# Optimization experiments

Measured on AMD Instinct MI355X. Metric: run time of the kernel, lower is better.

Reference implementation:

```python
import jax, jax.numpy as jnp
import numpy as np

N_NODES = 100000
N_EDGES = 1600000
D_IN = 128
D_HID = 128


def gcn_layer(x, src, dst, ew, W, b, n):
    """PyG GCNConv with normalize=True, add_self_loops=True (self-loop weight 1)."""
    h = x @ W  # [n, d_out]
    # degree includes self-loop weight 1.0
    deg = jax.ops.segment_sum(ew, dst, num_segments=n) + 1.0  # [n]
    dis = jnp.where(deg > 0, jax.lax.rsqrt(deg), 0.0)  # deg^{-1/2}
    norm = dis[src] * ew * dis[dst]  # [E]
    agg = jax.ops.segment_sum(norm[:, None] * h[src], dst, num_segments=n)
    # self-loop term: norm_ii = dis[i] * 1.0 * dis[i]
    agg = agg + (dis * dis)[:, None] * h
    return agg + b


def prelu(x, alpha):
    return jnp.where(x >= 0, x, alpha * x)


def setup_inputs() -> dict:
    key = jax.random.key(0)
    ks = jax.random.split(key, 12)
    x = jax.random.normal(ks[0], (N_NODES, D_IN), dtype=jnp.float32)
    edge_index = jax.random.randint(ks[1], (2, N_EDGES), 0, N_NODES, dtype=jnp.int64)
    edge_weight = jax.random.uniform(ks[2], (N_EDGES,), dtype=jnp.float32)
    s1 = 1.0 / np.sqrt(D_IN)
    s2 = 1.0 / np.sqrt(D_HID)
    params = {
        "W1": jax.random.normal(ks[3], (D_IN, D_HID), dtype=jnp.float32) * s1,
        "b1": jnp.zeros((D_HID,), dtype=jnp.float32),
        "a1": jnp.full((D_HID,), 0.25, dtype=jnp.float32),
        "W2": jax.random.normal(ks[4], (D_HID, D_HID), dtype=jnp.float32) * s2,
        "b2": jnp.zeros((D_HID,), dtype=jnp.float32),
        "a2": jnp.full((D_HID,), 0.25, dtype=jnp.float32),
        "W3": jax.random.normal(ks[5], (D_HID, D_HID), dtype=jnp.float32) * s2,
        "b3": jnp.zeros((D_HID,), dtype=jnp.float32),
        "a3": jnp.full((D_HID,), 0.25, dtype=jnp.float32),
    }
    return {"x": x, "edge_index": edge_index, "edge_weight": edge_weight, **params}


def reference(x, edge_index, edge_weight, W1, b1, a1, W2, b2, a2, W3, b3, a3):
    src, dst = edge_index[0], edge_index[1]
    n = x.shape[0]
    h = prelu(gcn_layer(x, src, dst, edge_weight, W1, b1, n), a1)
    h = prelu(gcn_layer(h, src, dst, edge_weight, W2, b2, n), a2)
    h = prelu(gcn_layer(h, src, dst, edge_weight, W3, b3, n), a3)
    return h
```

## Files before the change

kernel.cpp:

```cpp
#include <hip/hip_runtime.h>

#define N_NODES 100000
#define N_EDGES 1600000
#define D 128
#define TILE_ROWS 32
#define N_TILES (N_NODES / TILE_ROWS)
#define GEMM_BLOCKS 512
#define CHUNK 4096
#define NC ((N_EDGES + CHUNK - 1) / CHUNK)
#define NB ((N_NODES + 255) / 256)
#define HLEN (NB * NC)
#define SCAN_BLK ((HLEN + 1023) / 1024)

typedef unsigned int uint;
typedef unsigned long long u64;
typedef short short8 __attribute__((ext_vector_type(8)));
typedef float f32x4 __attribute__((ext_vector_type(4)));

__device__ inline ushort f2bf(float f) {
    union { float f; uint u; } v; v.f = f;
    uint r = v.u + 0x7fffu + ((v.u >> 16) & 1u);
    return (ushort)(r >> 16);
}
__device__ inline float bf2f(ushort b) {
    union { uint u; float f; } v; v.u = ((uint)b) << 16;
    return v.f;
}


__global__ __launch_bounds__(256) void k_hist(const int* __restrict__ dst, int* __restrict__ H) {
    __shared__ int hist[NB];
    int c = blockIdx.x;
    for (int i = threadIdx.x; i < NB; i += 256) hist[i] = 0;
    __syncthreads();
    int base = c * CHUNK;
    int lim = N_EDGES - base; if (lim > CHUNK) lim = CHUNK;
    for (int k = threadIdx.x; k < lim; k += 256)
        atomicAdd(&hist[dst[base + k] >> 8], 1);
    __syncthreads();
    for (int i = threadIdx.x; i < NB; i += 256) H[c * NB + i] = hist[i];
}

__global__ __launch_bounds__(256) void k_scanA(const int* __restrict__ H, int* __restrict__ HOFF,
                                               int* __restrict__ bsum) {
    __shared__ int sd[256];
    int t = threadIdx.x;
    int base = blockIdx.x * 1024 + t * 4;
    int v[4];
#pragma unroll
    for (int j = 0; j < 4; ++j) {
        int l = base + j;
        v[j] = (l < HLEN) ? H[(l % NC) * NB + (l / NC)] : 0;
    }
    int lsum = v[0] + v[1] + v[2] + v[3];
    sd[t] = lsum;
    __syncthreads();
    for (int off = 1; off < 256; off <<= 1) {
        int x = (t >= off) ? sd[t - off] : 0;
        __syncthreads();
        sd[t] += x;
        __syncthreads();
    }
    int excl = sd[t] - lsum;
    if (base + 0 < HLEN) HOFF[base + 0] = excl;
    if (base + 1 < HLEN) HOFF[base + 1] = excl + v[0];
    if (base + 2 < HLEN) HOFF[base + 2] = excl + v[0] + v[1];
    if (base + 3 < HLEN) HOFF[base + 3] = excl + v[0] + v[1] + v[2];
    if (t == 255) bsum[blockIdx.x] = sd[255];
}

__global__ __launch_bounds__(256) void k_scanB(int* __restrict__ bsum) {
    __shared__ int sd[256];
    int t = threadIdx.x;
    int v = (t < SCAN_BLK) ? bsum[t] : 0;
    sd[t] = v;
    __syncthreads();
    for (int off = 1; off < 256; off <<= 1) {
        int x = (t >= off) ? sd[t - off] : 0;
        __syncthreads();
        sd[t] += x;
        __syncthreads();
    }
    if (t < SCAN_BLK) bsum[t] = sd[t] - v;
}

__global__ void k_scanC(int* __restrict__ HOFF, const int* __restrict__ bsum) {
    int i = blockIdx.x * blockDim.x + threadIdx.x;
    if (i < HLEN) HOFF[i] += bsum[i >> 10];
}

__global__ __launch_bounds__(256) void k_pscat(const int* __restrict__ src, const int* __restrict__ dst,
                                               const float* __restrict__ ew, const int* __restrict__ HOFF,
                                               u64* __restrict__ tmp) {
    __shared__ int cur[NB];
    int c = blockIdx.x;
    for (int i = threadIdx.x; i < NB; i += 256) cur[i] = HOFF[i * NC + c];
    __syncthreads();
    int base = c * CHUNK;
    int lim = N_EDGES - base; if (lim > CHUNK) lim = CHUNK;
    for (int k = threadIdx.x; k < lim; k += 256) {
        int e = base + k;
        int s = src[e], t = dst[e];
        u64 q = (u64)llrintf(ew[e] * 1073741824.0f);
        int pos = atomicAdd(&cur[t >> 8], 1);
        tmp[pos] = (u64)s | ((u64)t << 17) | (q << 34);
    }
}

__global__ __launch_bounds__(256) void k_b1(const int* __restrict__ HOFF, const u64* __restrict__ tmp,
                                            float* __restrict__ dis, int* __restrict__ rowptr) {
    __shared__ int cnt[256];
    __shared__ u64 degq[256];
    __shared__ int sd[256];
    __shared__ int sbeg, send;
    int b = blockIdx.x, t = threadIdx.x;
    cnt[t] = 0; degq[t] = 0;
    if (t == 0) {
        sbeg = HOFF[b * NC];
        send = (b + 1 < NB) ? HOFF[(b + 1) * NC] : N_EDGES;
    }
    __syncthreads();
    int beg = sbeg, end = send, lo = b << 8;
    for (int e = beg + t; e < end; e += 256) {
        u64 r = tmp[e];
        int loc = (int)((r >> 17) & 0x1FFFF) - lo;
        atomicAdd(&cnt[loc], 1);
        atomicAdd(&degq[loc], r >> 34);
    }
    __syncthreads();
    int n = lo + t;
    if (n < N_NODES) {
        float deg = (float)((double)degq[t] * (1.0 / 1073741824.0));
        dis[n] = rsqrtf(deg + 1.0f);
    }
    int v = cnt[t];
    sd[t] = v;
    __syncthreads();
    for (int off = 1; off < 256; off <<= 1) {
        int x = (t >= off) ? sd[t - off] : 0;
        __syncthreads();
        sd[t] += x;
        __syncthreads();
    }
    if (n < N_NODES) rowptr[n] = beg + sd[t] - v;
    if (b == NB - 1 && t == 0) rowptr[N_NODES] = N_EDGES;
}

__global__ __launch_bounds__(256) void k_b2(const int* __restrict__ HOFF, const u64* __restrict__ tmp,
                                            const float* __restrict__ dis, const int* __restrict__ rowptr,
                                            int2* __restrict__ edges) {
    __shared__ int cur[256];
    __shared__ float disl[256];
    __shared__ int sbeg, send;
    int b = blockIdx.x, t = threadIdx.x;
    int lo = b << 8;
    int n = lo + t;
    cur[t] = (n < N_NODES) ? rowptr[n] : 0;
    disl[t] = (n < N_NODES) ? dis[n] : 0.0f;
    if (t == 0) {
        sbeg = HOFF[b * NC];
        send = (b + 1 < NB) ? HOFF[(b + 1) * NC] : N_EDGES;
    }
    __syncthreads();
    for (int e = sbeg + t; e < send; e += 256) {
        u64 r = tmp[e];
        int s = (int)(r & 0x1FFFF);
        int loc = (int)((r >> 17) & 0x1FFFF) - lo;
        float w = (float)(r >> 34) * (1.0f / 1073741824.0f);
        float coef = dis[s] * w * disl[loc];
        int pos = atomicAdd(&cur[loc], 1);
        edges[pos] = make_int2(s, __float_as_int(coef));
    }
}

__global__ void k_wsplit3(const float* __restrict__ W1, const float* __restrict__ W2,
                          const float* __restrict__ W3, ushort* __restrict__ wsp) {
    int gid = blockIdx.x * 256 + threadIdx.x;
    int l = gid >> 14;
    int i = gid & 16383;
    const float* W = (l == 0) ? W1 : (l == 1) ? W2 : W3;
    ushort* Wht = wsp + l * 32768;
    ushort* Wlt = Wht + 16384;
    int k = i >> 7, c = i & 127;
    float w = W[i];
    ushort wh = f2bf(w);
    ushort wl = f2bf(w - bf2f(wh));
    int j = k >> 3;
    int off = c * 128 + (((j ^ (c & 7)) << 3) | (k & 7));
    Wht[off] = wh;
    Wlt[off] = wl;
}

__global__ __launch_bounds__(256) void k_gemm_mfma(
    const float* __restrict__ x, const ushort* __restrict__ Wht,
    const ushort* __restrict__ Wlt, ushort* __restrict__ hb)
{
    __shared__ ushort WH[16384];
    __shared__ ushort WL[16384];
    __shared__ ushort XH[4096];
    __shared__ ushort XL[4096];

    const int tx = threadIdx.x;

    for (int i = tx; i < 2048; i += 256) {
        ((uint4*)WH)[i] = ((const uint4*)Wht)[i];
        ((uint4*)WL)[i] = ((const uint4*)Wlt)[i];
    }

    const int wv = tx >> 6;
    const int lane = tx & 63;
    const int lr = lane & 15;
    const int g = lane >> 4;
    const int c0 = wv * 32 + lr;
    const int c1 = c0 + 16;

    const int xr = (tx * 2) >> 4;
    const int xjb = (tx * 2) & 15;

    for (int tile = blockIdx.x; tile < N_TILES; tile += GEMM_BLOCKS) {
        const int row0 = tile * TILE_ROWS;
        __syncthreads();

        {
            const float* xp = x + (size_t)(row0 + xr) * D;
#pragma unroll
            for (int c = 0; c < 2; ++c) {
                int j = xjb + c;
                float4 a0 = *(const float4*)(xp + j * 8);
                float4 a1 = *(const float4*)(xp + j * 8 + 4);
                float v[8] = {a0.x, a0.y, a0.z, a0.w, a1.x, a1.y, a1.z, a1.w};
                uint4 uh, ul;
                uint* ph = (uint*)&uh; uint* pl = (uint*)&ul;
#pragma unroll
                for (int e = 0; e < 4; ++e) {
                    ushort h0 = f2bf(v[2 * e]),     h1 = f2bf(v[2 * e + 1]);
                    ushort l0 = f2bf(v[2 * e] - bf2f(h0));
                    ushort l1 = f2bf(v[2 * e + 1] - bf2f(h1));
                    ph[e] = (uint)h0 | ((uint)h1 << 16);
                    pl[e] = (uint)l0 | ((uint)l1 << 16);
                }
                int off = xr * 16 + (j ^ (xr & 7));
                ((uint4*)XH)[off] = uh;
                ((uint4*)XL)[off] = ul;
            }
        }
        __syncthreads();

        f32x4 acc[2][2] = {};
#pragma unroll
        for (int ks = 0; ks < 4; ++ks) {
            int co = ((ks * 4 + g) ^ (lr & 7)) << 3;
            short8 ah0 = *(short8*)&XH[lr * 128 + co];
            short8 ah1 = *(short8*)&XH[(16 + lr) * 128 + co];
            short8 al0 = *(short8*)&XL[lr * 128 + co];
            short8 al1 = *(short8*)&XL[(16 + lr) * 128 + co];
            short8 bh0 = *(short8*)&WH[c0 * 128 + co];
            short8 bh1 = *(short8*)&WH[c1 * 128 + co];
            short8 bl0 = *(short8*)&WL[c0 * 128 + co];
            short8 bl1 = *(short8*)&WL[c1 * 128 + co];

            acc[0][0] = __builtin_amdgcn_mfma_f32_16x16x32_bf16(ah0, bh0, acc[0][0], 0, 0, 0);
            acc[0][1] = __builtin_amdgcn_mfma_f32_16x16x32_bf16(ah0, bh1, acc[0][1], 0, 0, 0);
            acc[1][0] = __builtin_amdgcn_mfma_f32_16x16x32_bf16(ah1, bh0, acc[1][0], 0, 0, 0);
            acc[1][1] = __builtin_amdgcn_mfma_f32_16x16x32_bf16(ah1, bh1, acc[1][1], 0, 0, 0);
            acc[0][0] = __builtin_amdgcn_mfma_f32_16x16x32_bf16(al0, bh0, acc[0][0], 0, 0, 0);
            acc[0][1] = __builtin_amdgcn_mfma_f32_16x16x32_bf16(al0, bh1, acc[0][1], 0, 0, 0);
            acc[1][0] = __builtin_amdgcn_mfma_f32_16x16x32_bf16(al1, bh0, acc[1][0], 0, 0, 0);
            acc[1][1] = __builtin_amdgcn_mfma_f32_16x16x32_bf16(al1, bh1, acc[1][1], 0, 0, 0);
            acc[0][0] = __builtin_amdgcn_mfma_f32_16x16x32_bf16(ah0, bl0, acc[0][0], 0, 0, 0);
            acc[0][1] = __builtin_amdgcn_mfma_f32_16x16x32_bf16(ah0, bl1, acc[0][1], 0, 0, 0);
            acc[1][0] = __builtin_amdgcn_mfma_f32_16x16x32_bf16(ah1, bl0, acc[1][0], 0, 0, 0);
            acc[1][1] = __builtin_amdgcn_mfma_f32_16x16x32_bf16(ah1, bl1, acc[1][1], 0, 0, 0);
        }

#pragma unroll
        for (int rt = 0; rt < 2; ++rt) {
#pragma unroll
            for (int ct = 0; ct < 2; ++ct) {
                int colb = wv * 32 + ct * 16 + lr;
#pragma unroll
                for (int e = 0; e < 4; ++e) {
                    int row = row0 + rt * 16 + g * 4 + e;
                    hb[(size_t)row * D + colb] = f2bf(acc[rt][ct][e]);
                }
            }
        }
    }
}

__global__ __launch_bounds__(256) void k_gather(
    const int* __restrict__ rowptr, const int2* __restrict__ edges,
    const ushort* __restrict__ hb, const float* __restrict__ dis,
    const float* __restrict__ b, const float* __restrict__ alpha,
    float* __restrict__ out)
{
    int gid = blockIdx.x * 256 + threadIdx.x;
    int n = gid >> 6;
    if (n >= N_NODES) return;
    int lane = gid & 63;
    int q = lane >> 4;
    int c0 = (lane & 15) * 8;

    int beg = rowptr[n], end = rowptr[n + 1];
    float acc[8] = {0.f, 0.f, 0.f, 0.f, 0.f, 0.f, 0.f, 0.f};

    int e = beg + q;
    for (; e + 4 < end; e += 8) {
        int2 sc0 = edges[e];
        int2 sc1 = edges[e + 4];
        uint4 hv0 = *(const uint4*)&hb[(size_t)sc0.x * D + c0];
        uint4 hv1 = *(const uint4*)&hb[(size_t)sc1.x * D + c0];
        float ca = __int_as_float(sc0.y);
        float cb = __int_as_float(sc1.y);
#pragma unroll
        for (int j = 0; j < 4; ++j) {
            uint w0 = ((const uint*)&hv0)[j];
            uint w1 = ((const uint*)&hv1)[j];
            acc[2 * j]     = fmaf(ca, __uint_as_float(w0 << 16),         acc[2 * j]);
            acc[2 * j + 1] = fmaf(ca, __uint_as_float(w0 & 0xffff0000u), acc[2 * j + 1]);
            acc[2 * j]     = fmaf(cb, __uint_as_float(w1 << 16),         acc[2 * j]);
            acc[2 * j + 1] = fmaf(cb, __uint_as_float(w1 & 0xffff0000u), acc[2 * j + 1]);
        }
    }
    if (e < end) {
        int2 sc = edges[e];
        float c = __int_as_float(sc.y);
        uint4 hv = *(const uint4*)&hb[(size_t)sc.x * D + c0];
#pragma unroll
        for (int j = 0; j < 4; ++j) {
            uint w = ((const uint*)&hv)[j];
            acc[2 * j]     = fmaf(c, __uint_as_float(w << 16),         acc[2 * j]);
            acc[2 * j + 1] = fmaf(c, __uint_as_float(w & 0xffff0000u), acc[2 * j + 1]);
        }
    }

#pragma unroll
    for (int j = 0; j < 8; ++j) {
        acc[j] += __shfl_xor(acc[j], 16);
        acc[j] += __shfl_xor(acc[j], 32);
    }

    if (q == 0) {
        float di = dis[n];
        float d2 = di * di;
        uint4 hv = *(const uint4*)&hb[(size_t)n * D + c0];
        float r[8];
#pragma unroll
        for (int j = 0; j < 4; ++j) {
            uint w = ((const uint*)&hv)[j];
            float lo = __uint_as_float(w << 16);
            float hi = __uint_as_float(w & 0xffff0000u);
            r[2 * j]     = acc[2 * j]     + d2 * lo + b[c0 + 2 * j];
            r[2 * j + 1] = acc[2 * j + 1] + d2 * hi + b[c0 + 2 * j + 1];
        }
#pragma unroll
        for (int j = 0; j < 8; ++j) {
            float av = alpha[c0 + j];
            r[j] = r[j] >= 0.f ? r[j] : av * r[j];
        }
        *(float4*)&out[(size_t)n * D + c0]     = make_float4(r[0], r[1], r[2], r[3]);
        *(float4*)&out[(size_t)n * D + c0 + 4] = make_float4(r[4], r[5], r[6], r[7]);
    }
}


extern "C" void kernel_launch(void* const* d_in, const int* in_sizes, int n_in,
                              void* d_out, int out_size, void* d_ws, size_t ws_size,
                              hipStream_t stream) {
    const float* x   = (const float*)d_in[0];
    const int*   ei  = (const int*)d_in[1];
    const float* ew  = (const float*)d_in[2];
    const float* W1  = (const float*)d_in[3];
    const float* b1  = (const float*)d_in[4];
    const float* a1  = (const float*)d_in[5];
    const float* W2  = (const float*)d_in[6];
    const float* b2  = (const float*)d_in[7];
    const float* a2  = (const float*)d_in[8];
    const float* W3  = (const float*)d_in[9];
    const float* b3  = (const float*)d_in[10];
    const float* a3  = (const float*)d_in[11];

    const int* src = ei;
    const int* dst = ei + N_EDGES;

    float* out = (float*)d_out;

    ushort* hb    = (ushort*)d_ws;
    int2*   edges = (int2*)(hb + (size_t)N_NODES * D);
    u64*    tmp   = (u64*)(edges + N_EDGES);
    int*    H     = (int*)(tmp + N_EDGES);
    int*    HOFF  = H + HLEN;
    int*    bsum  = HOFF + HLEN;
    float*  dis   = (float*)(bsum + 256);
    int*    rowptr= (int*)(dis + N_NODES);
    ushort* wsp   = (ushort*)(rowptr + N_NODES + 2);
    ushort* Wht1 = wsp;             ushort* Wlt1 = wsp + 16384;
    ushort* Wht2 = wsp + 32768;     ushort* Wlt2 = wsp + 32768 + 16384;
    ushort* Wht3 = wsp + 65536;     ushort* Wlt3 = wsp + 65536 + 16384;

    k_wsplit3<<<192, 256, 0, stream>>>(W1, W2, W3, wsp);

    k_hist<<<NC, 256, 0, stream>>>(dst, H);
    k_scanA<<<SCAN_BLK, 256, 0, stream>>>(H, HOFF, bsum);
    k_scanB<<<1, 256, 0, stream>>>(bsum);
    k_scanC<<<(HLEN + 255) / 256, 256, 0, stream>>>(HOFF, bsum);
    k_pscat<<<NC, 256, 0, stream>>>(src, dst, ew, HOFF, tmp);
    k_b1<<<NB, 256, 0, stream>>>(HOFF, tmp, dis, rowptr);
    k_b2<<<NB, 256, 0, stream>>>(HOFF, tmp, dis, rowptr, edges);

    const int gather_blocks = (N_NODES * 64) / 256;

    k_gemm_mfma<<<GEMM_BLOCKS, 256, 0, stream>>>(x, Wht1, Wlt1, hb);
    k_gather<<<gather_blocks, 256, 0, stream>>>(rowptr, edges, hb, dis, b1, a1, out);
    k_gemm_mfma<<<GEMM_BLOCKS, 256, 0, stream>>>(out, Wht2, Wlt2, hb);
    k_gather<<<gather_blocks, 256, 0, stream>>>(rowptr, edges, hb, dis, b2, a2, out);
    k_gemm_mfma<<<GEMM_BLOCKS, 256, 0, stream>>>(out, Wht3, Wlt3, hb);
    k_gather<<<gather_blocks, 256, 0, stream>>>(rowptr, edges, hb, dis, b3, a3, out);
}
```

Baseline: 384.3 us.

## Fuse CSR build passes, pre-scale GEMM output by dis, sort edges by source bucket

Merges the two CSR-construction kernels into one, caching a block's packed edges in LDS so the temp buffer is read once when they fit. Within each destination row, edges are grouped by source-index bucket so neighbour gathers hit nearby rows of h. dis[src] is folded into the GEMM epilogue (h scaled by dis per row), which removes the random dis[s] load from edge coefficient construction and simplifies the self-loop term. The cost is larger LDS use (about 60KB) with lower occupancy, and one extra bf16 rounding of the scaled values.

```diff
diff --git a/kernel.cpp b/kernel.cpp
--- a/kernel.cpp
+++ b/kernel.cpp
@@ -11,6 +11,10 @@
 #define NB ((N_NODES + 255) / 256)
 #define HLEN (NB * NC)
 #define SCAN_BLK ((HLEN + 1023) / 1024)
+#define SB_SHIFT 13
+#define NSB 13
+#define SBP 17
+#define EBUF 5120
 
 typedef unsigned int uint;
 typedef unsigned long long u64;
@@ -107,34 +111,47 @@
     }
 }
 
-__global__ __launch_bounds__(256) void k_b1(const int* __restrict__ HOFF, const u64* __restrict__ tmp,
-                                            float* __restrict__ dis, int* __restrict__ rowptr) {
-    __shared__ int cnt[256];
+__global__ __launch_bounds__(256) void k_bfused(const int* __restrict__ HOFF, const u64* __restrict__ tmp,
+                                                float* __restrict__ dis, int* __restrict__ rowptr,
+                                                int2* __restrict__ edges) {
+    __shared__ u64 ebuf[EBUF];
     __shared__ u64 degq[256];
+    __shared__ int cnt2[256][SBP];
     __shared__ int sd[256];
-    __shared__ int sbeg, send;
+    __shared__ float disl[256];
     int b = blockIdx.x, t = threadIdx.x;
-    cnt[t] = 0; degq[t] = 0;
-    if (t == 0) {
-        sbeg = HOFF[b * NC];
-        send = (b + 1 < NB) ? HOFF[(b + 1) * NC] : N_EDGES;
-    }
-    __syncthreads();
-    int beg = sbeg, end = send, lo = b << 8;
+    int beg = HOFF[b * NC];
+    int end = (b + 1 < NB) ? HOFF[(b + 1) * NC] : N_EDGES;
+    int total = end - beg;
+    bool fit = (total <= EBUF);
+    degq[t] = 0;
+#pragma unroll
+    for (int j = 0; j < SBP; ++j) cnt2[t][j] = 0;
+    __syncthreads();
+    int lo = b << 8;
+
     for (int e = beg + t; e < end; e += 256) {
         u64 r = tmp[e];
+        if (fit) ebuf[e - beg] = r;
         int loc = (int)((r >> 17) & 0x1FFFF) - lo;
-        atomicAdd(&cnt[loc], 1);
+        int sb = (int)(r & 0x1FFFF) >> SB_SHIFT;
+        atomicAdd(&cnt2[loc][sb], 1);
         atomicAdd(&degq[loc], r >> 34);
     }
     __syncthreads();
+
     int n = lo + t;
+    float dv = 0.0f;
     if (n < N_NODES) {
         float deg = (float)((double)degq[t] * (1.0 / 1073741824.0));
-        dis[n] = rsqrtf(deg + 1.0f);
-    }
-    int v = cnt[t];
-    sd[t] = v;
+        dv = rsqrtf(deg + 1.0f);
+        dis[n] = dv;
+    }
+    disl[t] = dv;
+    int tot = 0;
+#pragma unroll
+    for (int j = 0; j < NSB; ++j) tot += cnt2[t][j];
+    sd[t] = tot;
     __syncthreads();
     for (int off = 1; off < 256; off <<= 1) {
         int x = (t >= off) ? sd[t - off] : 0;
@@ -142,34 +159,36 @@
         sd[t] += x;
         __syncthreads();
     }
-    if (n < N_NODES) rowptr[n] = beg + sd[t] - v;
+    int nbase = beg + sd[t] - tot;
+    if (n < N_NODES) rowptr[n] = nbase;
     if (b == NB - 1 && t == 0) rowptr[N_NODES] = N_EDGES;
-}
-
-__global__ __launch_bounds__(256) void k_b2(const int* __restrict__ HOFF, const u64* __restrict__ tmp,
-                                            const float* __restrict__ dis, const int* __restrict__ rowptr,
-                                            int2* __restrict__ edges) {
-    __shared__ int cur[256];
-    __shared__ float disl[256];
-    __shared__ int sbeg, send;
-    int b = blockIdx.x, t = threadIdx.x;
-    int lo = b << 8;
-    int n = lo + t;
-    cur[t] = (n < N_NODES) ? rowptr[n] : 0;
-    disl[t] = (n < N_NODES) ? dis[n] : 0.0f;
-    if (t == 0) {
-        sbeg = HOFF[b * NC];
-        send = (b + 1 < NB) ? HOFF[(b + 1) * NC] : N_EDGES;
-    }
-    __syncthreads();
-    for (int e = sbeg + t; e < send; e += 256) {
-        u64 r = tmp[e];
-        int s = (int)(r & 0x1FFFF);
-        int loc = (int)((r >> 17) & 0x1FFFF) - lo;
-        float w = (float)(r >> 34) * (1.0f / 1073741824.0f);
-        float coef = dis[s] * w * disl[loc];
-        int pos = atomicAdd(&cur[loc], 1);
-        edges[pos] = make_int2(s, __float_as_int(coef));
+    {
+        int run = nbase;
+#pragma unroll
+        for (int j = 0; j < NSB; ++j) { int c = cnt2[t][j]; cnt2[t][j] = run; run += c; }
+    }
+    __syncthreads();
+
+    if (fit) {
+        for (int i = t; i < total; i += 256) {
+            u64 r = ebuf[i];
+            int s = (int)(r & 0x1FFFF);
+            int loc = (int)((r >> 17) & 0x1FFFF) - lo;
+            float w = (float)(r >> 34) * (1.0f / 1073741824.0f);
+            float cf = w * disl[loc];
+            int pos = atomicAdd(&cnt2[loc][s >> SB_SHIFT], 1);
+            edges[pos] = make_int2(s, __float_as_int(cf));
+        }
+    } else {
+        for (int e = beg + t; e < end; e += 256) {
+            u64 r = tmp[e];
+            int s = (int)(r & 0x1FFFF);
+            int loc = (int)((r >> 17) & 0x1FFFF) - lo;
+            float w = (float)(r >> 34) * (1.0f / 1073741824.0f);
+            float cf = w * disl[loc];
+            int pos = atomicAdd(&cnt2[loc][s >> SB_SHIFT], 1);
+            edges[pos] = make_int2(s, __float_as_int(cf));
+        }
     }
 }
 
@@ -193,7 +212,8 @@
 
 __global__ __launch_bounds__(256) void k_gemm_mfma(
     const float* __restrict__ x, const ushort* __restrict__ Wht,
-    const ushort* __restrict__ Wlt, ushort* __restrict__ hb)
+    const ushort* __restrict__ Wlt, const float* __restrict__ dis,
+    ushort* __restrict__ hb)
 {
     __shared__ ushort WH[16384];
     __shared__ ushort WL[16384];
@@ -275,13 +295,15 @@
 
 #pragma unroll
         for (int rt = 0; rt < 2; ++rt) {
+            float4 dvq = *(const float4*)&dis[row0 + rt * 16 + g * 4];
+            const float dvv[4] = {dvq.x, dvq.y, dvq.z, dvq.w};
 #pragma unroll
             for (int ct = 0; ct < 2; ++ct) {
                 int colb = wv * 32 + ct * 16 + lr;
 #pragma unroll
                 for (int e = 0; e < 4; ++e) {
                     int row = row0 + rt * 16 + g * 4 + e;
-                    hb[(size_t)row * D + colb] = f2bf(acc[rt][ct][e]);
+                    hb[(size_t)row * D + colb] = f2bf(dvv[e] * acc[rt][ct][e]);
                 }
             }
         }
@@ -342,7 +364,6 @@
 
     if (q == 0) {
         float di = dis[n];
-        float d2 = di * di;
         uint4 hv = *(const uint4*)&hb[(size_t)n * D + c0];
         float r[8];
 #pragma unroll
@@ -350,8 +371,8 @@
             uint w = ((const uint*)&hv)[j];
             float lo = __uint_as_float(w << 16);
             float hi = __uint_as_float(w & 0xffff0000u);
-            r[2 * j]     = acc[2 * j]     + d2 * lo + b[c0 + 2 * j];
-            r[2 * j + 1] = acc[2 * j + 1] + d2 * hi + b[c0 + 2 * j + 1];
+            r[2 * j]     = acc[2 * j]     + di * lo + b[c0 + 2 * j];
+            r[2 * j + 1] = acc[2 * j + 1] + di * hi + b[c0 + 2 * j + 1];
         }
 #pragma unroll
         for (int j = 0; j < 8; ++j) {
@@ -385,15 +406,16 @@
 
     float* out = (float*)d_out;
 
-    ushort* hb    = (ushort*)d_ws;
-    int2*   edges = (int2*)(hb + (size_t)N_NODES * D);
-    u64*    tmp   = (u64*)(edges + N_EDGES);
-    int*    H     = (int*)(tmp + N_EDGES);
-    int*    HOFF  = H + HLEN;
-    int*    bsum  = HOFF + HLEN;
-    float*  dis   = (float*)(bsum + 256);
-    int*    rowptr= (int*)(dis + N_NODES);
-    ushort* wsp   = (ushort*)(rowptr + N_NODES + 2);
+    char* base = (char*)d_ws;
+    ushort* hb    = (ushort*)(base);
+    int2*   edges = (int2*)(base + 25600000);
+    u64*    tmp   = (u64*)(base + 38400000);
+    float*  dis   = (float*)(base + 51200000);
+    int*    H     = (int*)(base + 51600000);
+    int*    HOFF  = (int*)(base + 52211536);
+    int*    bsum  = (int*)(base + 52823072);
+    int*    rowptr= (int*)(base + 52824096);
+    ushort* wsp   = (ushort*)(base + 53224112);
     ushort* Wht1 = wsp;             ushort* Wlt1 = wsp + 16384;
     ushort* Wht2 = wsp + 32768;     ushort* Wlt2 = wsp + 32768 + 16384;
     ushort* Wht3 = wsp + 65536;     ushort* Wlt3 = wsp + 65536 + 16384;
@@ -405,15 +427,14 @@
     k_scanB<<<1, 256, 0, stream>>>(bsum);
     k_scanC<<<(HLEN + 255) / 256, 256, 0, stream>>>(HOFF, bsum);
     k_pscat<<<NC, 256, 0, stream>>>(src, dst, ew, HOFF, tmp);
-    k_b1<<<NB, 256, 0, stream>>>(HOFF, tmp, dis, rowptr);
-    k_b2<<<NB, 256, 0, stream>>>(HOFF, tmp, dis, rowptr, edges);
+    k_bfused<<<NB, 256, 0, stream>>>(HOFF, tmp, dis, rowptr, edges);
 
     const int gather_blocks = (N_NODES * 64) / 256;
 
-    k_gemm_mfma<<<GEMM_BLOCKS, 256, 0, stream>>>(x, Wht1, Wlt1, hb);
+    k_gemm_mfma<<<GEMM_BLOCKS, 256, 0, stream>>>(x, Wht1, Wlt1, dis, hb);
     k_gather<<<gather_blocks, 256, 0, stream>>>(rowptr, edges, hb, dis, b1, a1, out);
-    k_gemm_mfma<<<GEMM_BLOCKS, 256, 0, stream>>>(out, Wht2, Wlt2, hb);
+    k_gemm_mfma<<<GEMM_BLOCKS, 256, 0, stream>>>(out, Wht2, Wlt2, dis, hb);
     k_gather<<<gather_blocks, 256, 0, stream>>>(rowptr, edges, hb, dis, b2, a2, out);
-    k_gemm_mfma<<<GEMM_BLOCKS, 256, 0, stream>>>(out, Wht3, Wlt3, hb);
+    k_gemm_mfma<<<GEMM_BLOCKS, 256, 0, stream>>>(out, Wht3, Wlt3, dis, hb);
     k_gather<<<gather_blocks, 256, 0, stream>>>(rowptr, edges, hb, dis, b3, a3, out);
 }
```

Measured after the change: 378.9 us. About the same (-1.4%).
